# Performance work log

Hardware: AMD Instinct MI355X
Metric: run time of the kernel (lower is better)

Reference implementation:

```python
import jax, jax.numpy as jnp
import numpy as np

NUM_SPECIES = 16
INPUT_DIM = 256
HIDDEN_DIM = 512
MSG_DIM = 16
VOCAB = 64
A, B = 512, 32


def setup_inputs() -> dict:
    key = jax.random.key(0)
    ks = jax.random.split(key, 8)
    H = HIDDEN_DIM
    return {
        "x": jax.random.normal(ks[0], (A, B, INPUT_DIM), dtype=jnp.float32),
        "species_indices": jax.random.randint(ks[1], (A,), 0, NUM_SPECIES),
        # SpeciesLinear input_proj: weight (S, H, I), bias (S, H)
        "w_in": jax.random.normal(ks[2], (NUM_SPECIES, H, INPUT_DIM), dtype=jnp.float32) * 0.1,
        "b_in": jnp.zeros((NUM_SPECIES, H), dtype=jnp.float32),
        # LSTM (num_layers=1), PyTorch gate order: i, f, g, o
        "w_ih": jax.random.normal(ks[3], (4 * H, H), dtype=jnp.float32) * 0.04,
        "w_hh": jax.random.normal(ks[4], (4 * H, H), dtype=jnp.float32) * 0.04,
        "b_ih": jnp.zeros((4 * H,), dtype=jnp.float32),
        "b_hh": jnp.zeros((4 * H,), dtype=jnp.float32),
        # SpeciesLinear output_proj: weight (S, M*V, H), bias (S, M*V)
        "w_out": jax.random.normal(ks[5], (NUM_SPECIES, MSG_DIM * VOCAB, H), dtype=jnp.float32) * 0.1,
        "b_out": jnp.zeros((NUM_SPECIES, MSG_DIM * VOCAB), dtype=jnp.float32),
    }


def reference(x, species_indices, w_in, b_in, w_ih, w_hh, b_ih, b_hh, w_out, b_out):
    H = HIDDEN_DIM
    a, b, _ = x.shape
    # SpeciesLinear input projection + ReLU: gather per-agent weights then batched matmul
    wi = w_in[species_indices]              # (A, H, I)
    bi = b_in[species_indices]              # (A, H)
    x_proj = jax.nn.relu(jnp.einsum('abi,ahi->abh', x, wi) + bi[:, None, :])
    # Single-timestep LSTM with zero initial state (hidden=None path)
    xs = x_proj.reshape(a * b, H)
    gates = xs @ w_ih.T + b_ih + b_hh       # h0 == 0 so w_hh term vanishes mathematically,
    # but include it explicitly for faithfulness (zeros contribute nothing):
    h0 = jnp.zeros((a * b, H), dtype=x.dtype)
    c0 = jnp.zeros((a * b, H), dtype=x.dtype)
    gates = gates + h0 @ w_hh.T
    gi, gf, gg, go = jnp.split(gates, 4, axis=-1)
    i = jax.nn.sigmoid(gi)
    f = jax.nn.sigmoid(gf)
    g = jnp.tanh(gg)
    o = jax.nn.sigmoid(go)
    c1 = f * c0 + i * g
    h1 = o * jnp.tanh(c1)
    lstm_out = h1.reshape(a, b, H)
    # SpeciesLinear output projection
    wo = w_out[species_indices]             # (A, M*V, H)
    bo = b_out[species_indices]             # (A, M*V)
    logits = jnp.einsum('abh,aoh->abo', lstm_out, wo) + bo[:, None, :]
    logits = logits.reshape(a, b, MSG_DIM, VOCAB)
    h_out = h1[None, :, :]                  # (num_layers=1, A*B, H)
    c_out = c1[None, :, :]
    return (logits, h_out, c_out)
```

## Files before the change

kernel.cpp:

```cpp
#include <hip/hip_runtime.h>
#include <hip/hip_bf16.h>
#include <stdint.h>

#define NSPEC 16
#define IN_DIM 256
#define HID 512
#define ODIM 1024
#define NA 512
#define NB 32
#define NROWS (NA*NB)
#define NSLOTS 144

typedef __bf16 bf16x8 __attribute__((ext_vector_type(8)));
typedef float f32x4 __attribute__((ext_vector_type(4)));

__device__ __forceinline__ uint32_t f2bf1(float f){
  uint32_t u = __builtin_bit_cast(uint32_t, f);
  u += 0x7FFFu + ((u >> 16) & 1u);
  return u >> 16;
}
__device__ __forceinline__ uint32_t pack2(float a, float b){
  return f2bf1(a) | (f2bf1(b) << 16);
}
__device__ __forceinline__ uint4 load8_pack(const float* __restrict__ src){
  float4 f0 = *reinterpret_cast<const float4*>(src);
  float4 f1 = *reinterpret_cast<const float4*>(src + 4);
  uint4 v;
  v.x = pack2(f0.x, f0.y); v.y = pack2(f0.z, f0.w);
  v.z = pack2(f1.x, f1.y); v.w = pack2(f1.z, f1.w);
  return v;
}
__device__ __forceinline__ float sigm(float x){ return 1.0f / (1.0f + __expf(-x)); }

__global__ void k_prep(const int* __restrict__ sp, int* __restrict__ order,
                       int* __restrict__ slot_s, int* __restrict__ slot_st,
                       int* __restrict__ slot_na){
  __shared__ int cnt[NSPEC], off[NSPEC], cur[NSPEC];
  int t = threadIdx.x;
  if (t < NSPEC) cnt[t] = 0;
  __syncthreads();
  int s = sp[t];
  atomicAdd(&cnt[s], 1);
  __syncthreads();
  if (t == 0){
    int o = 0;
    for (int i = 0; i < NSPEC; i++){ off[i] = o; cur[i] = o; o += cnt[i]; }
  }
  __syncthreads();
  int pos = atomicAdd(&cur[s], 1);
  order[pos] = t;
  __syncthreads();
  if (t == 0){
    int k = 0;
    for (int i = 0; i < NSPEC; i++){
      int c = cnt[i], st = off[i];
      for (int j = 0; j < c; j += 4){
        slot_s[k] = i; slot_st[k] = st + j;
        slot_na[k] = (c - j < 4) ? (c - j) : 4; k++;
      }
    }
    for (; k < NSLOTS; k++){ slot_s[k] = 0; slot_st[k] = 0; slot_na[k] = 0; }
  }
}

__global__ __launch_bounds__(256) void k_xproj(
    const float* __restrict__ x, const float* __restrict__ w_in,
    const float* __restrict__ b_in,
    const int* __restrict__ order, const int* __restrict__ slot_s,
    const int* __restrict__ slot_st, const int* __restrict__ slot_na,
    ushort* __restrict__ xproj)
{
  int slot = blockIdx.y;
  int na = slot_na[slot];
  if (na == 0) return;
  int spec = slot_s[slot];
  int start = slot_st[slot];
  int n0 = blockIdx.x * 128;
  int tid = threadIdx.x, lane = tid & 63, wid = tid >> 6;
  int mh = wid >> 1, nh = wid & 1;

  __shared__ uint4 ldsA[128 * 8];
  __shared__ uint4 ldsB[128 * 8];

  int arow[4];
#pragma unroll
  for (int i = 0; i < 4; i++) arow[i] = (i < na) ? order[start + i] : 0;

  f32x4 acc[4][4];
#pragma unroll
  for (int i = 0; i < 4; i++)
#pragma unroll
    for (int j = 0; j < 4; j++) acc[i][j] = (f32x4){0.f, 0.f, 0.f, 0.f};

  for (int ch = 0; ch < 4; ++ch){
    int k0 = ch * 64;
#pragma unroll
    for (int i = 0; i < 4; i++){
      int u = tid + i * 256;
      int r = u >> 3, uu = u & 7;
      int ai = r >> 5;
      uint4 v = {0u, 0u, 0u, 0u};
      if (ai < na){
        const float* src = x + ((size_t)(arow[ai] * NB + (r & 31))) * IN_DIM + k0 + uu * 8;
        v = load8_pack(src);
      }
      ldsA[r * 8 + (uu ^ (r & 7))] = v;
    }
#pragma unroll
    for (int i = 0; i < 4; i++){
      int u = tid + i * 256;
      int r = u >> 3, uu = u & 7;
      const float* src = w_in + ((size_t)(spec * HID + n0 + r)) * IN_DIM + k0 + uu * 8;
      ldsB[r * 8 + (uu ^ (r & 7))] = load8_pack(src);
    }
    __syncthreads();
#pragma unroll
    for (int kk = 0; kk < 2; ++kk){
      int lr = lane & 15, lk = (lane >> 4) + kk * 4;
      bf16x8 af[4], bfr[4];
#pragma unroll
      for (int mt = 0; mt < 4; mt++){
        int r = mh * 64 + mt * 16 + lr;
        af[mt] = __builtin_bit_cast(bf16x8, ldsA[r * 8 + (lk ^ (r & 7))]);
      }
#pragma unroll
      for (int nt = 0; nt < 4; nt++){
        int r = nh * 64 + nt * 16 + lr;
        bfr[nt] = __builtin_bit_cast(bf16x8, ldsB[r * 8 + (lk ^ (r & 7))]);
      }
#pragma unroll
      for (int mt = 0; mt < 4; mt++)
#pragma unroll
        for (int nt = 0; nt < 4; nt++)
          acc[mt][nt] = __builtin_amdgcn_mfma_f32_16x16x32_bf16(af[mt], bfr[nt], acc[mt][nt], 0, 0, 0);
    }
    __syncthreads();
  }
  int lr = lane & 15;
#pragma unroll
  for (int mt = 0; mt < 4; mt++){
    int rbase = mh * 64 + mt * 16 + ((lane >> 4) << 2);
#pragma unroll
    for (int j = 0; j < 4; j++){
      int r = rbase + j;
      int ai = r >> 5;
      if (ai >= na) continue;
      size_t grow = (size_t)(arow[ai] * NB + (r & 31));
#pragma unroll
      for (int nt = 0; nt < 4; nt++){
        int col = n0 + nh * 64 + nt * 16 + lr;
        float v = acc[mt][nt][j] + b_in[spec * HID + col];
        v = v > 0.f ? v : 0.f;
        xproj[grow * HID + col] = (ushort)f2bf1(v);
      }
    }
  }
}

__global__ __launch_bounds__(256) void k_lstm(
    const ushort* __restrict__ xproj, const float* __restrict__ w_ih,
    const float* __restrict__ b_ih, const float* __restrict__ b_hh,
    float* __restrict__ hout, float* __restrict__ cout_)
{
  int n0 = blockIdx.x * 32;
  int m0 = blockIdx.y * 128;
  int tid = threadIdx.x, lane = tid & 63, wid = tid >> 6;

  __shared__ uint4 ldsA[128 * 8];
  __shared__ uint4 ldsB[96 * 8];

  f32x4 acc[2][6];
#pragma unroll
  for (int i = 0; i < 2; i++)
#pragma unroll
    for (int j = 0; j < 6; j++) acc[i][j] = (f32x4){0.f, 0.f, 0.f, 0.f};

  for (int ch = 0; ch < 8; ++ch){
    int k0 = ch * 64;
#pragma unroll
    for (int i = 0; i < 4; i++){
      int u = tid + i * 256;
      int r = u >> 3, uu = u & 7;
      const uint4* src = reinterpret_cast<const uint4*>(xproj + (size_t)(m0 + r) * HID + k0 + uu * 8);
      ldsA[r * 8 + (uu ^ (r & 7))] = *src;
    }
#pragma unroll
    for (int i = 0; i < 3; i++){
      int u = tid + i * 256;
      int r = u >> 3, uu = u & 7;
      int gate = r >> 5;
      int gbase = (gate == 0) ? 0 : ((gate == 1) ? 1024 : 1536);
      const float* src = w_ih + (size_t)(gbase + n0 + (r & 31)) * HID + k0 + uu * 8;
      ldsB[r * 8 + (uu ^ (r & 7))] = load8_pack(src);
    }
    __syncthreads();
#pragma unroll
    for (int kk = 0; kk < 2; ++kk){
      int lr = lane & 15, lk = (lane >> 4) + kk * 4;
      bf16x8 af[2], bfr[6];
#pragma unroll
      for (int mt = 0; mt < 2; mt++){
        int r = wid * 32 + mt * 16 + lr;
        af[mt] = __builtin_bit_cast(bf16x8, ldsA[r * 8 + (lk ^ (r & 7))]);
      }
#pragma unroll
      for (int gn = 0; gn < 6; gn++){
        int r = gn * 16 + lr;
        bfr[gn] = __builtin_bit_cast(bf16x8, ldsB[r * 8 + (lk ^ (r & 7))]);
      }
#pragma unroll
      for (int mt = 0; mt < 2; mt++)
#pragma unroll
        for (int gn = 0; gn < 6; gn++)
          acc[mt][gn] = __builtin_amdgcn_mfma_f32_16x16x32_bf16(af[mt], bfr[gn], acc[mt][gn], 0, 0, 0);
    }
    __syncthreads();
  }
  int lr = lane & 15;
#pragma unroll
  for (int mt = 0; mt < 2; mt++){
    int rbase = m0 + wid * 32 + mt * 16 + ((lane >> 4) << 2);
#pragma unroll
    for (int ntg = 0; ntg < 2; ntg++){
      int c = n0 + ntg * 16 + lr;
      float bi0 = b_ih[c]        + b_hh[c];
      float bi1 = b_ih[1024 + c] + b_hh[1024 + c];
      float bi2 = b_ih[1536 + c] + b_hh[1536 + c];
#pragma unroll
      for (int j = 0; j < 4; j++){
        float gi = acc[mt][0 + ntg][j] + bi0;
        float gg = acc[mt][2 + ntg][j] + bi1;
        float go = acc[mt][4 + ntg][j] + bi2;
        float iv = sigm(gi);
        float gv = tanhf(gg);
        float ov = sigm(go);
        float c1 = iv * gv;
        float h1 = ov * tanhf(c1);
        size_t idx = (size_t)(rbase + j) * HID + c;
        hout[idx] = h1;
        cout_[idx] = c1;
      }
    }
  }
}

__global__ __launch_bounds__(256) void k_logits(
    const float* __restrict__ h1, const float* __restrict__ w_out,
    const float* __restrict__ b_out,
    const int* __restrict__ order, const int* __restrict__ slot_s,
    const int* __restrict__ slot_st, const int* __restrict__ slot_na,
    float* __restrict__ logits)
{
  int slot = blockIdx.y;
  int na = slot_na[slot];
  if (na == 0) return;
  int spec = slot_s[slot];
  int start = slot_st[slot];
  int n0 = blockIdx.x * 128;
  int tid = threadIdx.x, lane = tid & 63, wid = tid >> 6;
  int mh = wid >> 1, nh = wid & 1;

  __shared__ uint4 ldsA[128 * 8];
  __shared__ uint4 ldsB[128 * 8];

  int arow[4];
#pragma unroll
  for (int i = 0; i < 4; i++) arow[i] = (i < na) ? order[start + i] : 0;

  f32x4 acc[4][4];
#pragma unroll
  for (int i = 0; i < 4; i++)
#pragma unroll
    for (int j = 0; j < 4; j++) acc[i][j] = (f32x4){0.f, 0.f, 0.f, 0.f};

  for (int ch = 0; ch < 8; ++ch){
    int k0 = ch * 64;
#pragma unroll
    for (int i = 0; i < 4; i++){
      int u = tid + i * 256;
      int r = u >> 3, uu = u & 7;
      int ai = r >> 5;
      uint4 v = {0u, 0u, 0u, 0u};
      if (ai < na){
        const float* src = h1 + ((size_t)(arow[ai] * NB + (r & 31))) * HID + k0 + uu * 8;
        v = load8_pack(src);
      }
      ldsA[r * 8 + (uu ^ (r & 7))] = v;
    }
#pragma unroll
    for (int i = 0; i < 4; i++){
      int u = tid + i * 256;
      int r = u >> 3, uu = u & 7;
      const float* src = w_out + ((size_t)(spec * ODIM + n0 + r)) * HID + k0 + uu * 8;
      ldsB[r * 8 + (uu ^ (r & 7))] = load8_pack(src);
    }
    __syncthreads();
#pragma unroll
    for (int kk = 0; kk < 2; ++kk){
      int lr = lane & 15, lk = (lane >> 4) + kk * 4;
      bf16x8 af[4], bfr[4];
#pragma unroll
      for (int mt = 0; mt < 4; mt++){
        int r = mh * 64 + mt * 16 + lr;
        af[mt] = __builtin_bit_cast(bf16x8, ldsA[r * 8 + (lk ^ (r & 7))]);
      }
#pragma unroll
      for (int nt = 0; nt < 4; nt++){
        int r = nh * 64 + nt * 16 + lr;
        bfr[nt] = __builtin_bit_cast(bf16x8, ldsB[r * 8 + (lk ^ (r & 7))]);
      }
#pragma unroll
      for (int mt = 0; mt < 4; mt++)
#pragma unroll
        for (int nt = 0; nt < 4; nt++)
          acc[mt][nt] = __builtin_amdgcn_mfma_f32_16x16x32_bf16(af[mt], bfr[nt], acc[mt][nt], 0, 0, 0);
    }
    __syncthreads();
  }
  int lr = lane & 15;
#pragma unroll
  for (int mt = 0; mt < 4; mt++){
    int rbase = mh * 64 + mt * 16 + ((lane >> 4) << 2);
#pragma unroll
    for (int j = 0; j < 4; j++){
      int r = rbase + j;
      int ai = r >> 5;
      if (ai >= na) continue;
      size_t grow = (size_t)(arow[ai] * NB + (r & 31));
#pragma unroll
      for (int nt = 0; nt < 4; nt++){
        int col = n0 + nh * 64 + nt * 16 + lr;
        float v = acc[mt][nt][j] + b_out[spec * ODIM + col];
        logits[grow * ODIM + col] = v;
      }
    }
  }
}

extern "C" void kernel_launch(void* const* d_in, const int* in_sizes, int n_in,
                              void* d_out, int out_size, void* d_ws, size_t ws_size,
                              hipStream_t stream){
  const float* x     = (const float*)d_in[0];
  const int*   sp    = (const int*)  d_in[1];
  const float* w_in  = (const float*)d_in[2];
  const float* b_in  = (const float*)d_in[3];
  const float* w_ih  = (const float*)d_in[4];
  const float* b_ih  = (const float*)d_in[6];
  const float* b_hh  = (const float*)d_in[7];
  const float* w_out = (const float*)d_in[8];
  const float* b_out = (const float*)d_in[9];

  float* out    = (float*)d_out;
  float* logits = out;
  float* hout   = out + (size_t)NROWS * ODIM;
  float* cout_  = hout + (size_t)NROWS * HID;
  ushort* xproj = (ushort*)d_out;

  int* order   = (int*)d_ws;
  int* slot_s  = order + NA;
  int* slot_st = slot_s + NSLOTS;
  int* slot_na = slot_st + NSLOTS;

  k_prep<<<1, 512, 0, stream>>>(sp, order, slot_s, slot_st, slot_na);
  k_xproj<<<dim3(4, NSLOTS), 256, 0, stream>>>(x, w_in, b_in, order, slot_s, slot_st, slot_na, xproj);
  k_lstm<<<dim3(16, 128), 256, 0, stream>>>(xproj, w_ih, b_ih, b_hh, hout, cout_);
  k_logits<<<dim3(8, NSLOTS), 256, 0, stream>>>(hout, w_out, b_out, order, slot_s, slot_st, slot_na, logits);
}
```

Measured before the change: 332.6 us.

## Pre-convert weights to pre-swizzled bf16 and load tiles via global_load_lds

Adds a conversion kernel that turns w_in, the used w_ih gate rows and, when workspace allows, w_out into bf16 with the LDS XOR swizzle already applied. The GEMM kernels can then copy tiles straight into LDS with global_load_lds instead of converting fp32 per tile. xproj is also written pre-swizzled, and the LSTM tile is enlarged to 128x64 per block to reuse more data. The conversion runs on every call and adds its own pass over the weights. Correctness depends on the swizzle matching the lane-to-LDS layout that global_load_lds uses.

```diff
diff --git a/kernel.cpp b/kernel.cpp
--- a/kernel.cpp
+++ b/kernel.cpp
@@ -1,5 +1,4 @@
 #include <hip/hip_runtime.h>
-#include <hip/hip_bf16.h>
 #include <stdint.h>
 
 #define NSPEC 16
@@ -13,6 +12,10 @@
 
 typedef __bf16 bf16x8 __attribute__((ext_vector_type(8)));
 typedef float f32x4 __attribute__((ext_vector_type(4)));
+
+#define GLOAD16(g, l) __builtin_amdgcn_global_load_lds( \
+    (const __attribute__((address_space(1))) void*)(g), \
+    (__attribute__((address_space(3))) void*)(l), 16, 0, 0)
 
 __device__ __forceinline__ uint32_t f2bf1(float f){
   uint32_t u = __builtin_bit_cast(uint32_t, f);
@@ -63,8 +66,41 @@
   }
 }
 
+__global__ __launch_bounds__(256) void k_conv(
+    const float* __restrict__ w_in, const float* __restrict__ w_ih,
+    const float* __restrict__ w_out,
+    ushort* __restrict__ wi, ushort* __restrict__ wg, ushort* __restrict__ wo,
+    int do_wo)
+{
+  const int U1 = NSPEC*HID*IN_DIM/8;
+  const int U2 = 3*HID*HID/8;
+  const int U3 = NSPEC*ODIM*HID/8;
+  int total = U1 + U2 + (do_wo ? U3 : 0);
+  for (int u = blockIdx.x*256 + threadIdx.x; u < total; u += gridDim.x*256){
+    const float* src; ushort* drow; int row, col;
+    if (u < U1){
+      int e = u*8; row = e >> 8; col = e & 255;
+      src = w_in + (size_t)row*IN_DIM + col;
+      drow = wi + (size_t)row*IN_DIM;
+    } else if (u < U1+U2){
+      int e = (u-U1)*8; row = e >> 9; col = e & 511;
+      int g = row >> 9;
+      int srow = (g==0 ? 0 : (g==1 ? 1024 : 1536)) + (row & 511);
+      src = w_ih + (size_t)srow*HID + col;
+      drow = wg + (size_t)row*HID;
+    } else {
+      int e = (u-U1-U2)*8; row = e >> 9; col = e & 511;
+      src = w_out + (size_t)row*HID + col;
+      drow = wo + (size_t)row*HID;
+    }
+    uint4 v = load8_pack(src);
+    int colp = (col & ~63) | ((((col >> 3) & 7) ^ (row & 7)) << 3);
+    *reinterpret_cast<uint4*>(drow + colp) = v;
+  }
+}
+
 __global__ __launch_bounds__(256) void k_xproj(
-    const float* __restrict__ x, const float* __restrict__ w_in,
+    const float* __restrict__ x, const ushort* __restrict__ wi,
     const float* __restrict__ b_in,
     const int* __restrict__ order, const int* __restrict__ slot_s,
     const int* __restrict__ slot_st, const int* __restrict__ slot_na,
@@ -78,6 +114,7 @@
   int n0 = blockIdx.x * 128;
   int tid = threadIdx.x, lane = tid & 63, wid = tid >> 6;
   int mh = wid >> 1, nh = wid & 1;
+  int lrow = lane >> 3, lseg = lane & 7;
 
   __shared__ uint4 ldsA[128 * 8];
   __shared__ uint4 ldsB[128 * 8];
@@ -108,10 +145,9 @@
     }
 #pragma unroll
     for (int i = 0; i < 4; i++){
-      int u = tid + i * 256;
-      int r = u >> 3, uu = u & 7;
-      const float* src = w_in + ((size_t)(spec * HID + n0 + r)) * IN_DIM + k0 + uu * 8;
-      ldsB[r * 8 + (uu ^ (r & 7))] = load8_pack(src);
+      int rr = wid * 32 + i * 8 + lrow;
+      const ushort* bsrc = wi + (size_t)(spec * HID + n0 + rr) * IN_DIM + k0 + lseg * 8;
+      GLOAD16(bsrc, &ldsB[(wid * 32 + i * 8) * 8]);
     }
     __syncthreads();
 #pragma unroll
@@ -145,71 +181,72 @@
       int r = rbase + j;
       int ai = r >> 5;
       if (ai >= na) continue;
-      size_t grow = (size_t)(arow[ai] * NB + (r & 31));
+      int grow = arow[ai] * NB + (r & 31);
 #pragma unroll
       for (int nt = 0; nt < 4; nt++){
         int col = n0 + nh * 64 + nt * 16 + lr;
         float v = acc[mt][nt][j] + b_in[spec * HID + col];
         v = v > 0.f ? v : 0.f;
-        xproj[grow * HID + col] = (ushort)f2bf1(v);
+        int colp = (col & ~63) | ((((col >> 3) & 7) ^ (grow & 7)) << 3) | (col & 7);
+        xproj[(size_t)grow * HID + colp] = (ushort)f2bf1(v);
       }
     }
   }
 }
 
 __global__ __launch_bounds__(256) void k_lstm(
-    const ushort* __restrict__ xproj, const float* __restrict__ w_ih,
+    const ushort* __restrict__ xproj, const ushort* __restrict__ wg,
     const float* __restrict__ b_ih, const float* __restrict__ b_hh,
     float* __restrict__ hout, float* __restrict__ cout_)
 {
-  int n0 = blockIdx.x * 32;
+  int n0 = blockIdx.x * 64;
   int m0 = blockIdx.y * 128;
   int tid = threadIdx.x, lane = tid & 63, wid = tid >> 6;
+  int mh = wid >> 1, nh = wid & 1;
+  int lrow = lane >> 3, lseg = lane & 7;
 
   __shared__ uint4 ldsA[128 * 8];
-  __shared__ uint4 ldsB[96 * 8];
-
-  f32x4 acc[2][6];
-#pragma unroll
-  for (int i = 0; i < 2; i++)
+  __shared__ uint4 ldsB[192 * 8];
+
+  f32x4 acc[4][6];
+#pragma unroll
+  for (int i = 0; i < 4; i++)
 #pragma unroll
     for (int j = 0; j < 6; j++) acc[i][j] = (f32x4){0.f, 0.f, 0.f, 0.f};
 
   for (int ch = 0; ch < 8; ++ch){
     int k0 = ch * 64;
+    const ushort* asrc = xproj + (size_t)(m0 + wid * 32 + lrow) * HID + k0 + lseg * 8;
 #pragma unroll
     for (int i = 0; i < 4; i++){
-      int u = tid + i * 256;
-      int r = u >> 3, uu = u & 7;
-      const uint4* src = reinterpret_cast<const uint4*>(xproj + (size_t)(m0 + r) * HID + k0 + uu * 8);
-      ldsA[r * 8 + (uu ^ (r & 7))] = *src;
-    }
-#pragma unroll
-    for (int i = 0; i < 3; i++){
-      int u = tid + i * 256;
-      int r = u >> 3, uu = u & 7;
-      int gate = r >> 5;
-      int gbase = (gate == 0) ? 0 : ((gate == 1) ? 1024 : 1536);
-      const float* src = w_ih + (size_t)(gbase + n0 + (r & 31)) * HID + k0 + uu * 8;
-      ldsB[r * 8 + (uu ^ (r & 7))] = load8_pack(src);
+      GLOAD16(asrc + (size_t)i * 8 * HID, &ldsA[(wid * 32 + i * 8) * 8]);
+    }
+#pragma unroll
+    for (int i = 0; i < 6; i++){
+      int rr = wid * 48 + i * 8 + lrow;
+      int g = rr >> 6;
+      const ushort* bsrc = wg + (size_t)(g * HID + n0 + (rr & 63)) * HID + k0 + lseg * 8;
+      GLOAD16(bsrc, &ldsB[(wid * 48 + i * 8) * 8]);
     }
     __syncthreads();
 #pragma unroll
     for (int kk = 0; kk < 2; ++kk){
       int lr = lane & 15, lk = (lane >> 4) + kk * 4;
-      bf16x8 af[2], bfr[6];
-#pragma unroll
-      for (int mt = 0; mt < 2; mt++){
-        int r = wid * 32 + mt * 16 + lr;
+      bf16x8 af[4], bfr[6];
+#pragma unroll
+      for (int mt = 0; mt < 4; mt++){
+        int r = mh * 64 + mt * 16 + lr;
         af[mt] = __builtin_bit_cast(bf16x8, ldsA[r * 8 + (lk ^ (r & 7))]);
       }
 #pragma unroll
-      for (int gn = 0; gn < 6; gn++){
-        int r = gn * 16 + lr;
-        bfr[gn] = __builtin_bit_cast(bf16x8, ldsB[r * 8 + (lk ^ (r & 7))]);
-      }
-#pragma unroll
-      for (int mt = 0; mt < 2; mt++)
+      for (int g = 0; g < 3; g++)
+#pragma unroll
+        for (int t = 0; t < 2; t++){
+          int rr = g * 64 + nh * 32 + t * 16 + lr;
+          bfr[g * 2 + t] = __builtin_bit_cast(bf16x8, ldsB[rr * 8 + (lk ^ (rr & 7))]);
+        }
+#pragma unroll
+      for (int mt = 0; mt < 4; mt++)
 #pragma unroll
         for (int gn = 0; gn < 6; gn++)
           acc[mt][gn] = __builtin_amdgcn_mfma_f32_16x16x32_bf16(af[mt], bfr[gn], acc[mt][gn], 0, 0, 0);
@@ -218,19 +255,19 @@
   }
   int lr = lane & 15;
 #pragma unroll
-  for (int mt = 0; mt < 2; mt++){
-    int rbase = m0 + wid * 32 + mt * 16 + ((lane >> 4) << 2);
-#pragma unroll
-    for (int ntg = 0; ntg < 2; ntg++){
-      int c = n0 + ntg * 16 + lr;
-      float bi0 = b_ih[c]        + b_hh[c];
-      float bi1 = b_ih[1024 + c] + b_hh[1024 + c];
-      float bi2 = b_ih[1536 + c] + b_hh[1536 + c];
+  for (int t = 0; t < 2; t++){
+    int c = n0 + nh * 32 + t * 16 + lr;
+    float bi0 = b_ih[c]        + b_hh[c];
+    float bi1 = b_ih[1024 + c] + b_hh[1024 + c];
+    float bi2 = b_ih[1536 + c] + b_hh[1536 + c];
+#pragma unroll
+    for (int mt = 0; mt < 4; mt++){
+      int rbase = m0 + mh * 64 + mt * 16 + ((lane >> 4) << 2);
 #pragma unroll
       for (int j = 0; j < 4; j++){
-        float gi = acc[mt][0 + ntg][j] + bi0;
-        float gg = acc[mt][2 + ntg][j] + bi1;
-        float go = acc[mt][4 + ntg][j] + bi2;
+        float gi = acc[mt][0 + t][j] + bi0;
+        float gg = acc[mt][2 + t][j] + bi1;
+        float go = acc[mt][4 + t][j] + bi2;
         float iv = sigm(gi);
         float gv = tanhf(gg);
         float ov = sigm(go);
@@ -244,9 +281,10 @@
   }
 }
 
+template<bool PRE>
 __global__ __launch_bounds__(256) void k_logits(
-    const float* __restrict__ h1, const float* __restrict__ w_out,
-    const float* __restrict__ b_out,
+    const float* __restrict__ h1, const ushort* __restrict__ wo,
+    const float* __restrict__ w_out, const float* __restrict__ b_out,
     const int* __restrict__ order, const int* __restrict__ slot_s,
     const int* __restrict__ slot_st, const int* __restrict__ slot_na,
     float* __restrict__ logits)
@@ -259,6 +297,7 @@
   int n0 = blockIdx.x * 128;
   int tid = threadIdx.x, lane = tid & 63, wid = tid >> 6;
   int mh = wid >> 1, nh = wid & 1;
+  int lrow = lane >> 3, lseg = lane & 7;
 
   __shared__ uint4 ldsA[128 * 8];
   __shared__ uint4 ldsB[128 * 8];
@@ -287,12 +326,21 @@
       }
       ldsA[r * 8 + (uu ^ (r & 7))] = v;
     }
-#pragma unroll
-    for (int i = 0; i < 4; i++){
-      int u = tid + i * 256;
-      int r = u >> 3, uu = u & 7;
-      const float* src = w_out + ((size_t)(spec * ODIM + n0 + r)) * HID + k0 + uu * 8;
-      ldsB[r * 8 + (uu ^ (r & 7))] = load8_pack(src);
+    if (PRE){
+#pragma unroll
+      for (int i = 0; i < 4; i++){
+        int rr = wid * 32 + i * 8 + lrow;
+        const ushort* bsrc = wo + (size_t)(spec * ODIM + n0 + rr) * HID + k0 + lseg * 8;
+        GLOAD16(bsrc, &ldsB[(wid * 32 + i * 8) * 8]);
+      }
+    } else {
+#pragma unroll
+      for (int i = 0; i < 4; i++){
+        int u = tid + i * 256;
+        int r = u >> 3, uu = u & 7;
+        const float* src = w_out + ((size_t)(spec * ODIM + n0 + r)) * HID + k0 + uu * 8;
+        ldsB[r * 8 + (uu ^ (r & 7))] = load8_pack(src);
+      }
     }
     __syncthreads();
 #pragma unroll
@@ -355,14 +403,24 @@
   float* hout   = out + (size_t)NROWS * ODIM;
   float* cout_  = hout + (size_t)NROWS * HID;
   ushort* xproj = (ushort*)d_out;
+  ushort* wi_bf = xproj + (size_t)NROWS * HID;
+  ushort* wg_bf = wi_bf + (size_t)NSPEC * HID * IN_DIM;
 
   int* order   = (int*)d_ws;
   int* slot_s  = order + NA;
   int* slot_st = slot_s + NSLOTS;
   int* slot_na = slot_st + NSLOTS;
-
-  k_prep<<<1, 512, 0, stream>>>(sp, order, slot_s, slot_st, slot_na);
-  k_xproj<<<dim3(4, NSLOTS), 256, 0, stream>>>(x, w_in, b_in, order, slot_s, slot_st, slot_na, xproj);
-  k_lstm<<<dim3(16, 128), 256, 0, stream>>>(xproj, w_ih, b_ih, b_hh, hout, cout_);
-  k_logits<<<dim3(8, NSLOTS), 256, 0, stream>>>(hout, w_out, b_out, order, slot_s, slot_st, slot_na, logits);
-}
+  ushort* wo_bf = (ushort*)((char*)d_ws + 4096);
+
+  size_t need = 4096 + (size_t)NSPEC * ODIM * HID * 2;
+  bool pre = ws_size >= need;
+
+  k_prep<<<1, NA, 0, stream>>>(sp, order, slot_s, slot_st, slot_na);
+  k_conv<<<1024, 256, 0, stream>>>(w_in, w_ih, w_out, wi_bf, wg_bf, wo_bf, pre ? 1 : 0);
+  k_xproj<<<dim3(4, NSLOTS), 256, 0, stream>>>(x, wi_bf, b_in, order, slot_s, slot_st, slot_na, xproj);
+  k_lstm<<<dim3(8, 128), 256, 0, stream>>>(xproj, wg_bf, b_ih, b_hh, hout, cout_);
+  if (pre)
+    k_logits<true><<<dim3(8, NSLOTS), 256, 0, stream>>>(hout, wo_bf, w_out, b_out, order, slot_s, slot_st, slot_na, logits);
+  else
+    k_logits<false><<<dim3(8, NSLOTS), 256, 0, stream>>>(hout, wo_bf, w_out, b_out, order, slot_s, slot_st, slot_na, logits);
+}
```

New measurement: 325.9 us. -2.0%, faster.

## Pre-convert inputs and weights to swizzled bf16 and stream them via global_load_lds

Applied to the files above, without the earlier changes.

A new conversion kernel packs x (gathered into slot order), w_in, the used w_ih gate rows and w_out into bf16 workspace buffers, pre-swizzled to match the LDS layout. The GEMM kernels then copy tiles straight to LDS with global_load_lds instead of loading fp32 and converting per block. The intermediates (xproj, h1) stay in slot-ordered, swizzled bf16, which removes gathers and the fp32 re-read of h1 in the logits stage. Blocks grow to 512 threads with larger N tiles and a swizzled block order. The cost is an extra full conversion pass over all weights on every call and more workspace traffic.

```diff
diff --git a/kernel.cpp b/kernel.cpp
--- a/kernel.cpp
+++ b/kernel.cpp
@@ -1,5 +1,4 @@
 #include <hip/hip_runtime.h>
-#include <hip/hip_bf16.h>
 #include <stdint.h>
 
 #define NSPEC 16
@@ -13,6 +12,10 @@
 
 typedef __bf16 bf16x8 __attribute__((ext_vector_type(8)));
 typedef float f32x4 __attribute__((ext_vector_type(4)));
+
+#define GLOAD16(g, l) __builtin_amdgcn_global_load_lds( \
+    (const __attribute__((address_space(1))) void*)(g), \
+    (__attribute__((address_space(3))) void*)(l), 16, 0, 0)
 
 __device__ __forceinline__ uint32_t f2bf1(float f){
   uint32_t u = __builtin_bit_cast(uint32_t, f);
@@ -63,70 +66,105 @@
   }
 }
 
-__global__ __launch_bounds__(256) void k_xproj(
+__global__ __launch_bounds__(256) void k_conv(
     const float* __restrict__ x, const float* __restrict__ w_in,
+    const float* __restrict__ w_ih, const float* __restrict__ w_out,
+    const int* __restrict__ order, const int* __restrict__ slot_st,
+    const int* __restrict__ slot_na,
+    ushort* __restrict__ xbf, ushort* __restrict__ wi,
+    ushort* __restrict__ wg, ushort* __restrict__ wo)
+{
+  const int UX  = NSLOTS*128*(IN_DIM/8);
+  const int UWI = NSPEC*HID*(IN_DIM/8);
+  const int UWG = 3*HID*(HID/8);
+  const int UWO = NSPEC*ODIM*(HID/8);
+  int total = UX + UWI + UWG + UWO;
+  for (int u = blockIdx.x*256 + threadIdx.x; u < total; u += gridDim.x*256){
+    uint4 v = {0u,0u,0u,0u};
+    ushort* dst;
+    if (u < UX){
+      int row = u >> 5, cu = u & 31;
+      int s = row >> 7, r = row & 127;
+      int cup = (cu & 24) | ((cu & 7) ^ (r & 7));
+      dst = xbf + ((size_t)row << 8) + (cup << 3);
+      if (r < slot_na[s]*32){
+        int arow = order[slot_st[s] + (r >> 5)];
+        v = load8_pack(x + ((size_t)(arow*NB + (r & 31)) << 8) + (cu << 3));
+      }
+    } else if (u < UX + UWI){
+      int t2 = u - UX; int row = t2 >> 5, cu = t2 & 31;
+      int cup = (cu & 24) | ((cu & 7) ^ (row & 7));
+      dst = wi + ((size_t)row << 8) + (cup << 3);
+      v = load8_pack(w_in + ((size_t)row << 8) + (cu << 3));
+    } else if (u < UX + UWI + UWG){
+      int t2 = u - UX - UWI; int row = t2 >> 6, cu = t2 & 63;
+      int g = row >> 9;
+      int srow = (g == 0 ? 0 : (g == 1 ? 1024 : 1536)) + (row & 511);
+      int cup = (cu & 56) | ((cu & 7) ^ (row & 7));
+      dst = wg + ((size_t)row << 9) + (cup << 3);
+      v = load8_pack(w_ih + ((size_t)srow << 9) + (cu << 3));
+    } else {
+      int t2 = u - UX - UWI - UWG; int row = t2 >> 6, cu = t2 & 63;
+      int cup = (cu & 56) | ((cu & 7) ^ (row & 7));
+      dst = wo + ((size_t)row << 9) + (cup << 3);
+      v = load8_pack(w_out + ((size_t)row << 9) + (cu << 3));
+    }
+    *reinterpret_cast<uint4*>(dst) = v;
+  }
+}
+
+__global__ __launch_bounds__(512) void k_xproj(
+    const ushort* __restrict__ xbf, const ushort* __restrict__ wi,
     const float* __restrict__ b_in,
-    const int* __restrict__ order, const int* __restrict__ slot_s,
-    const int* __restrict__ slot_st, const int* __restrict__ slot_na,
+    const int* __restrict__ slot_s, const int* __restrict__ slot_na,
     ushort* __restrict__ xproj)
 {
-  int slot = blockIdx.y;
+  int id = blockIdx.x;
+  int swz = (id & 7)*36 + (id >> 3);
+  int bx = swz & 1, slot = swz >> 1;
   int na = slot_na[slot];
   if (na == 0) return;
   int spec = slot_s[slot];
-  int start = slot_st[slot];
-  int n0 = blockIdx.x * 128;
+  int n0 = bx << 8;
   int tid = threadIdx.x, lane = tid & 63, wid = tid >> 6;
-  int mh = wid >> 1, nh = wid & 1;
-
-  __shared__ uint4 ldsA[128 * 8];
-  __shared__ uint4 ldsB[128 * 8];
-
-  int arow[4];
-#pragma unroll
-  for (int i = 0; i < 4; i++) arow[i] = (i < na) ? order[start + i] : 0;
+  int mh = wid >> 2, nh = wid & 3;
+  int lr = lane & 15, lq = lane >> 4;
+
+  __shared__ uint4 ldsA[128*8];
+  __shared__ uint4 ldsB[256*8];
 
   f32x4 acc[4][4];
 #pragma unroll
   for (int i = 0; i < 4; i++)
 #pragma unroll
-    for (int j = 0; j < 4; j++) acc[i][j] = (f32x4){0.f, 0.f, 0.f, 0.f};
+    for (int j = 0; j < 4; j++) acc[i][j] = (f32x4){0.f,0.f,0.f,0.f};
 
   for (int ch = 0; ch < 4; ++ch){
     int k0 = ch * 64;
 #pragma unroll
+    for (int i = 0; i < 2; i++){
+      int u = i*512 + tid; int row = u >> 3, seg = u & 7;
+      GLOAD16(xbf + (size_t)(slot*128 + row)*IN_DIM + k0 + seg*8, &ldsA[i*512 + wid*64]);
+    }
+#pragma unroll
     for (int i = 0; i < 4; i++){
-      int u = tid + i * 256;
-      int r = u >> 3, uu = u & 7;
-      int ai = r >> 5;
-      uint4 v = {0u, 0u, 0u, 0u};
-      if (ai < na){
-        const float* src = x + ((size_t)(arow[ai] * NB + (r & 31))) * IN_DIM + k0 + uu * 8;
-        v = load8_pack(src);
-      }
-      ldsA[r * 8 + (uu ^ (r & 7))] = v;
-    }
-#pragma unroll
-    for (int i = 0; i < 4; i++){
-      int u = tid + i * 256;
-      int r = u >> 3, uu = u & 7;
-      const float* src = w_in + ((size_t)(spec * HID + n0 + r)) * IN_DIM + k0 + uu * 8;
-      ldsB[r * 8 + (uu ^ (r & 7))] = load8_pack(src);
+      int u = i*512 + tid; int row = u >> 3, seg = u & 7;
+      GLOAD16(wi + (size_t)(spec*HID + n0 + row)*IN_DIM + k0 + seg*8, &ldsB[i*512 + wid*64]);
     }
     __syncthreads();
 #pragma unroll
     for (int kk = 0; kk < 2; ++kk){
-      int lr = lane & 15, lk = (lane >> 4) + kk * 4;
+      int lk = lq + kk*4;
       bf16x8 af[4], bfr[4];
 #pragma unroll
       for (int mt = 0; mt < 4; mt++){
-        int r = mh * 64 + mt * 16 + lr;
-        af[mt] = __builtin_bit_cast(bf16x8, ldsA[r * 8 + (lk ^ (r & 7))]);
+        int r = mh*64 + mt*16 + lr;
+        af[mt] = __builtin_bit_cast(bf16x8, ldsA[r*8 + (lk ^ (r & 7))]);
       }
 #pragma unroll
       for (int nt = 0; nt < 4; nt++){
-        int r = nh * 64 + nt * 16 + lr;
-        bfr[nt] = __builtin_bit_cast(bf16x8, ldsB[r * 8 + (lk ^ (r & 7))]);
+        int r = nh*64 + nt*16 + lr;
+        bfr[nt] = __builtin_bit_cast(bf16x8, ldsB[r*8 + (lk ^ (r & 7))]);
       }
 #pragma unroll
       for (int mt = 0; mt < 4; mt++)
@@ -136,178 +174,182 @@
     }
     __syncthreads();
   }
-  int lr = lane & 15;
 #pragma unroll
   for (int mt = 0; mt < 4; mt++){
-    int rbase = mh * 64 + mt * 16 + ((lane >> 4) << 2);
 #pragma unroll
     for (int j = 0; j < 4; j++){
-      int r = rbase + j;
-      int ai = r >> 5;
-      if (ai >= na) continue;
-      size_t grow = (size_t)(arow[ai] * NB + (r & 31));
+      int prl = mh*64 + mt*16 + lq*4 + j;
 #pragma unroll
       for (int nt = 0; nt < 4; nt++){
-        int col = n0 + nh * 64 + nt * 16 + lr;
-        float v = acc[mt][nt][j] + b_in[spec * HID + col];
+        int col = n0 + nh*64 + nt*16 + lr;
+        float v = acc[mt][nt][j] + b_in[spec*HID + col];
         v = v > 0.f ? v : 0.f;
-        xproj[grow * HID + col] = (ushort)f2bf1(v);
-      }
-    }
-  }
-}
-
-__global__ __launch_bounds__(256) void k_lstm(
-    const ushort* __restrict__ xproj, const float* __restrict__ w_ih,
+        int colp = (col & ~63) | ((((col >> 3) & 7) ^ (prl & 7)) << 3) | (col & 7);
+        xproj[(size_t)(slot*128 + prl)*HID + colp] = (ushort)f2bf1(v);
+      }
+    }
+  }
+}
+
+__global__ __launch_bounds__(512) void k_lstm(
+    const ushort* __restrict__ xproj, const ushort* __restrict__ wg,
     const float* __restrict__ b_ih, const float* __restrict__ b_hh,
-    float* __restrict__ hout, float* __restrict__ cout_)
+    const int* __restrict__ order, const int* __restrict__ slot_st,
+    const int* __restrict__ slot_na,
+    float* __restrict__ hout, float* __restrict__ cout_,
+    ushort* __restrict__ h1bf)
 {
-  int n0 = blockIdx.x * 32;
-  int m0 = blockIdx.y * 128;
+  int id = blockIdx.x;
+  int swz = (id & 7)*72 + (id >> 3);
+  int bx = swz & 3, slot = swz >> 2;
+  int na = slot_na[slot];
+  if (na == 0) return;
+  int st = slot_st[slot];
+  int n0 = bx << 7;
   int tid = threadIdx.x, lane = tid & 63, wid = tid >> 6;
-
-  __shared__ uint4 ldsA[128 * 8];
-  __shared__ uint4 ldsB[96 * 8];
-
-  f32x4 acc[2][6];
-#pragma unroll
-  for (int i = 0; i < 2; i++)
-#pragma unroll
-    for (int j = 0; j < 6; j++) acc[i][j] = (f32x4){0.f, 0.f, 0.f, 0.f};
+  int mh = wid >> 2, nh = wid & 3;
+  int lr = lane & 15, lq = lane >> 4;
+
+  int arow[4];
+#pragma unroll
+  for (int i = 0; i < 4; i++) arow[i] = (i < na) ? order[st + i] : 0;
+
+  __shared__ uint4 ldsA[128*8];
+  __shared__ uint4 ldsB[384*8];
+
+  f32x4 acc[4][6];
+#pragma unroll
+  for (int i = 0; i < 4; i++)
+#pragma unroll
+    for (int j = 0; j < 6; j++) acc[i][j] = (f32x4){0.f,0.f,0.f,0.f};
 
   for (int ch = 0; ch < 8; ++ch){
     int k0 = ch * 64;
 #pragma unroll
-    for (int i = 0; i < 4; i++){
-      int u = tid + i * 256;
-      int r = u >> 3, uu = u & 7;
-      const uint4* src = reinterpret_cast<const uint4*>(xproj + (size_t)(m0 + r) * HID + k0 + uu * 8);
-      ldsA[r * 8 + (uu ^ (r & 7))] = *src;
-    }
-#pragma unroll
-    for (int i = 0; i < 3; i++){
-      int u = tid + i * 256;
-      int r = u >> 3, uu = u & 7;
-      int gate = r >> 5;
-      int gbase = (gate == 0) ? 0 : ((gate == 1) ? 1024 : 1536);
-      const float* src = w_ih + (size_t)(gbase + n0 + (r & 31)) * HID + k0 + uu * 8;
-      ldsB[r * 8 + (uu ^ (r & 7))] = load8_pack(src);
+    for (int i = 0; i < 2; i++){
+      int u = i*512 + tid; int row = u >> 3, seg = u & 7;
+      GLOAD16(xproj + (size_t)(slot*128 + row)*HID + k0 + seg*8, &ldsA[i*512 + wid*64]);
+    }
+#pragma unroll
+    for (int i = 0; i < 6; i++){
+      int u = i*512 + tid; int rr = u >> 3, seg = u & 7;
+      int g = rr >> 7;
+      GLOAD16(wg + (size_t)(g*HID + n0 + (rr & 127))*HID + k0 + seg*8, &ldsB[i*512 + wid*64]);
     }
     __syncthreads();
 #pragma unroll
     for (int kk = 0; kk < 2; ++kk){
-      int lr = lane & 15, lk = (lane >> 4) + kk * 4;
-      bf16x8 af[2], bfr[6];
-#pragma unroll
-      for (int mt = 0; mt < 2; mt++){
-        int r = wid * 32 + mt * 16 + lr;
-        af[mt] = __builtin_bit_cast(bf16x8, ldsA[r * 8 + (lk ^ (r & 7))]);
-      }
-#pragma unroll
-      for (int gn = 0; gn < 6; gn++){
-        int r = gn * 16 + lr;
-        bfr[gn] = __builtin_bit_cast(bf16x8, ldsB[r * 8 + (lk ^ (r & 7))]);
-      }
-#pragma unroll
-      for (int mt = 0; mt < 2; mt++)
+      int lk = lq + kk*4;
+      bf16x8 af[4], bfr[6];
+#pragma unroll
+      for (int mt = 0; mt < 4; mt++){
+        int r = mh*64 + mt*16 + lr;
+        af[mt] = __builtin_bit_cast(bf16x8, ldsA[r*8 + (lk ^ (r & 7))]);
+      }
+#pragma unroll
+      for (int g = 0; g < 3; g++)
+#pragma unroll
+        for (int t = 0; t < 2; t++){
+          int rr = g*128 + nh*32 + t*16 + lr;
+          bfr[g*2 + t] = __builtin_bit_cast(bf16x8, ldsB[rr*8 + (lk ^ (rr & 7))]);
+        }
+#pragma unroll
+      for (int mt = 0; mt < 4; mt++)
 #pragma unroll
         for (int gn = 0; gn < 6; gn++)
           acc[mt][gn] = __builtin_amdgcn_mfma_f32_16x16x32_bf16(af[mt], bfr[gn], acc[mt][gn], 0, 0, 0);
     }
     __syncthreads();
   }
-  int lr = lane & 15;
-#pragma unroll
-  for (int mt = 0; mt < 2; mt++){
-    int rbase = m0 + wid * 32 + mt * 16 + ((lane >> 4) << 2);
-#pragma unroll
-    for (int ntg = 0; ntg < 2; ntg++){
-      int c = n0 + ntg * 16 + lr;
-      float bi0 = b_ih[c]        + b_hh[c];
-      float bi1 = b_ih[1024 + c] + b_hh[1024 + c];
-      float bi2 = b_ih[1536 + c] + b_hh[1536 + c];
+#pragma unroll
+  for (int t = 0; t < 2; t++){
+    int c = n0 + nh*32 + t*16 + lr;
+    float bi0 = b_ih[c]        + b_hh[c];
+    float bi1 = b_ih[1024 + c] + b_hh[1024 + c];
+    float bi2 = b_ih[1536 + c] + b_hh[1536 + c];
+#pragma unroll
+    for (int mt = 0; mt < 4; mt++){
 #pragma unroll
       for (int j = 0; j < 4; j++){
-        float gi = acc[mt][0 + ntg][j] + bi0;
-        float gg = acc[mt][2 + ntg][j] + bi1;
-        float go = acc[mt][4 + ntg][j] + bi2;
+        int prl = mh*64 + mt*16 + lq*4 + j;
+        float gi = acc[mt][0 + t][j] + bi0;
+        float gg = acc[mt][2 + t][j] + bi1;
+        float go = acc[mt][4 + t][j] + bi2;
         float iv = sigm(gi);
         float gv = tanhf(gg);
         float ov = sigm(go);
         float c1 = iv * gv;
         float h1 = ov * tanhf(c1);
-        size_t idx = (size_t)(rbase + j) * HID + c;
-        hout[idx] = h1;
-        cout_[idx] = c1;
-      }
-    }
-  }
-}
-
-__global__ __launch_bounds__(256) void k_logits(
-    const float* __restrict__ h1, const float* __restrict__ w_out,
+        int colp = (c & ~63) | ((((c >> 3) & 7) ^ (prl & 7)) << 3) | (c & 7);
+        h1bf[(size_t)(slot*128 + prl)*HID + colp] = (ushort)f2bf1(h1);
+        if (prl < na*32){
+          size_t grow = (size_t)(arow[prl >> 5]*NB + (prl & 31));
+          hout[grow*HID + c] = h1;
+          cout_[grow*HID + c] = c1;
+        }
+      }
+    }
+  }
+}
+
+__global__ __launch_bounds__(512) void k_logits(
+    const ushort* __restrict__ h1bf, const ushort* __restrict__ wo,
     const float* __restrict__ b_out,
     const int* __restrict__ order, const int* __restrict__ slot_s,
     const int* __restrict__ slot_st, const int* __restrict__ slot_na,
     float* __restrict__ logits)
 {
-  int slot = blockIdx.y;
+  int id = blockIdx.x;
+  int swz = (id & 7)*72 + (id >> 3);
+  int bx = swz & 3, slot = swz >> 2;
   int na = slot_na[slot];
   if (na == 0) return;
   int spec = slot_s[slot];
-  int start = slot_st[slot];
-  int n0 = blockIdx.x * 128;
+  int st = slot_st[slot];
+  int n0 = bx << 8;
   int tid = threadIdx.x, lane = tid & 63, wid = tid >> 6;
-  int mh = wid >> 1, nh = wid & 1;
-
-  __shared__ uint4 ldsA[128 * 8];
-  __shared__ uint4 ldsB[128 * 8];
+  int mh = wid >> 2, nh = wid & 3;
+  int lr = lane & 15, lq = lane >> 4;
 
   int arow[4];
 #pragma unroll
-  for (int i = 0; i < 4; i++) arow[i] = (i < na) ? order[start + i] : 0;
+  for (int i = 0; i < 4; i++) arow[i] = (i < na) ? order[st + i] : 0;
+
+  __shared__ uint4 ldsA[128*8];
+  __shared__ uint4 ldsB[256*8];
 
   f32x4 acc[4][4];
 #pragma unroll
   for (int i = 0; i < 4; i++)
 #pragma unroll
-    for (int j = 0; j < 4; j++) acc[i][j] = (f32x4){0.f, 0.f, 0.f, 0.f};
+    for (int j = 0; j < 4; j++) acc[i][j] = (f32x4){0.f,0.f,0.f,0.f};
 
   for (int ch = 0; ch < 8; ++ch){
     int k0 = ch * 64;
 #pragma unroll
+    for (int i = 0; i < 2; i++){
+      int u = i*512 + tid; int row = u >> 3, seg = u & 7;
+      GLOAD16(h1bf + (size_t)(slot*128 + row)*HID + k0 + seg*8, &ldsA[i*512 + wid*64]);
+    }
+#pragma unroll
     for (int i = 0; i < 4; i++){
-      int u = tid + i * 256;
-      int r = u >> 3, uu = u & 7;
-      int ai = r >> 5;
-      uint4 v = {0u, 0u, 0u, 0u};
-      if (ai < na){
-        const float* src = h1 + ((size_t)(arow[ai] * NB + (r & 31))) * HID + k0 + uu * 8;
-        v = load8_pack(src);
-      }
-      ldsA[r * 8 + (uu ^ (r & 7))] = v;
-    }
-#pragma unroll
-    for (int i = 0; i < 4; i++){
-      int u = tid + i * 256;
-      int r = u >> 3, uu = u & 7;
-      const float* src = w_out + ((size_t)(spec * ODIM + n0 + r)) * HID + k0 + uu * 8;
-      ldsB[r * 8 + (uu ^ (r & 7))] = load8_pack(src);
+      int u = i*512 + tid; int rr = u >> 3, seg = u & 7;
+      GLOAD16(wo + (size_t)(spec*ODIM + n0 + rr)*HID + k0 + seg*8, &ldsB[i*512 + wid*64]);
     }
     __syncthreads();
 #pragma unroll
     for (int kk = 0; kk < 2; ++kk){
-      int lr = lane & 15, lk = (lane >> 4) + kk * 4;
+      int lk = lq + kk*4;
       bf16x8 af[4], bfr[4];
 #pragma unroll
       for (int mt = 0; mt < 4; mt++){
-        int r = mh * 64 + mt * 16 + lr;
-        af[mt] = __builtin_bit_cast(bf16x8, ldsA[r * 8 + (lk ^ (r & 7))]);
+        int r = mh*64 + mt*16 + lr;
+        af[mt] = __builtin_bit_cast(bf16x8, ldsA[r*8 + (lk ^ (r & 7))]);
       }
 #pragma unroll
       for (int nt = 0; nt < 4; nt++){
-        int r = nh * 64 + nt * 16 + lr;
-        bfr[nt] = __builtin_bit_cast(bf16x8, ldsB[r * 8 + (lk ^ (r & 7))]);
+        int r = nh*64 + nt*16 + lr;
+        bfr[nt] = __builtin_bit_cast(bf16x8, ldsB[r*8 + (lk ^ (r & 7))]);
       }
 #pragma unroll
       for (int mt = 0; mt < 4; mt++)
@@ -317,21 +359,17 @@
     }
     __syncthreads();
   }
-  int lr = lane & 15;
 #pragma unroll
   for (int mt = 0; mt < 4; mt++){
-    int rbase = mh * 64 + mt * 16 + ((lane >> 4) << 2);
 #pragma unroll
     for (int j = 0; j < 4; j++){
-      int r = rbase + j;
-      int ai = r >> 5;
-      if (ai >= na) continue;
-      size_t grow = (size_t)(arow[ai] * NB + (r & 31));
+      int prl = mh*64 + mt*16 + lq*4 + j;
+      if (prl >= na*32) continue;
+      size_t grow = (size_t)(arow[prl >> 5]*NB + (prl & 31));
 #pragma unroll
       for (int nt = 0; nt < 4; nt++){
-        int col = n0 + nh * 64 + nt * 16 + lr;
-        float v = acc[mt][nt][j] + b_out[spec * ODIM + col];
-        logits[grow * ODIM + col] = v;
+        int col = n0 + nh*64 + nt*16 + lr;
+        logits[grow*ODIM + col] = acc[mt][nt][j] + b_out[spec*ODIM + col];
       }
     }
   }
@@ -354,15 +392,23 @@
   float* logits = out;
   float* hout   = out + (size_t)NROWS * ODIM;
   float* cout_  = hout + (size_t)NROWS * HID;
-  ushort* xproj = (ushort*)d_out;
 
   int* order   = (int*)d_ws;
   int* slot_s  = order + NA;
   int* slot_st = slot_s + NSLOTS;
   int* slot_na = slot_st + NSLOTS;
-
-  k_prep<<<1, 512, 0, stream>>>(sp, order, slot_s, slot_st, slot_na);
-  k_xproj<<<dim3(4, NSLOTS), 256, 0, stream>>>(x, w_in, b_in, order, slot_s, slot_st, slot_na, xproj);
-  k_lstm<<<dim3(16, 128), 256, 0, stream>>>(xproj, w_ih, b_ih, b_hh, hout, cout_);
-  k_logits<<<dim3(8, NSLOTS), 256, 0, stream>>>(hout, w_out, b_out, order, slot_s, slot_st, slot_na, logits);
-}
+  ushort* xbf   = (ushort*)((char*)d_ws + 4096);
+  ushort* xproj = xbf   + (size_t)NSLOTS*128*IN_DIM;
+  ushort* h1bf  = xproj + (size_t)NSLOTS*128*HID;
+  ushort* wi    = h1bf  + (size_t)NSLOTS*128*HID;
+  ushort* wg    = wi    + (size_t)NSPEC*HID*IN_DIM;
+  ushort* wo    = wg    + (size_t)3*HID*HID;
+
+  k_prep<<<1, NA, 0, stream>>>(sp, order, slot_s, slot_st, slot_na);
+  k_conv<<<1024, 256, 0, stream>>>(x, w_in, w_ih, w_out, order, slot_st, slot_na,
+                                   xbf, wi, wg, wo);
+  k_xproj<<<288, 512, 0, stream>>>(xbf, wi, b_in, slot_s, slot_na, xproj);
+  k_lstm<<<576, 512, 0, stream>>>(xproj, wg, b_ih, b_hh, order, slot_st, slot_na,
+                                  hout, cout_, h1bf);
+  k_logits<<<576, 512, 0, stream>>>(h1bf, wo, b_out, order, slot_s, slot_st, slot_na, logits);
+}
```

Result: slower. 358.6 us (+7.8%).
